# Kernel optimization log

Measured on AMD Instinct MI355X. Metric: run time of the kernel, lower is better.

Reference implementation:

```python
import jax, jax.numpy as jnp
import numpy as np

E = 1024   # embed_dim
H = 16     # num_heads
D = E // H # head_dim = 64
B = 2
S = 2048

def setup_inputs() -> dict:
    key = jax.random.key(0)
    ks = jax.random.split(key, 11)
    std = 0.02
    return {
        "query": jax.random.normal(ks[0], (B, S, E), jnp.float32),
        "key":   jax.random.normal(ks[1], (B, S, E), jnp.float32),
        "value": jax.random.normal(ks[2], (B, S, E), jnp.float32),
        "Wq": std * jax.random.normal(ks[3], (E, E), jnp.float32),
        "bq": jnp.zeros((E,), jnp.float32),
        "Wk": std * jax.random.normal(ks[4], (D, E), jnp.float32),
        "bk": jnp.zeros((D,), jnp.float32),
        "Wv": std * jax.random.normal(ks[5], (D, E), jnp.float32),
        "bv": jnp.zeros((D,), jnp.float32),
        "Wo": std * jax.random.normal(ks[6], (E, E), jnp.float32),
        "bo": jnp.zeros((E,), jnp.float32),
    }

def reference(query, key, value, Wq, bq, Wk, bk, Wv, bv, Wo, bo):
    b, t, _ = query.shape
    scaling = D ** -0.5
    q = query @ Wq.T + bq                      # [B, T, E]
    k = key @ Wk.T + bk                        # [B, S, D] (single shared KV head)
    v = value @ Wv.T + bv                      # [B, S, D]
    q = q.reshape(b, t, H, D).transpose(0, 2, 1, 3) * scaling  # [B, H, T, D]
    # MQA: broadcast shared k/v across heads inside einsum (no materialized expand)
    attn_weights = jnp.einsum("bhtd,bsd->bhts", q, k)          # [B, H, T, S]
    attn_probs = jax.nn.softmax(attn_weights, axis=-1)
    attn_output = jnp.einsum("bhts,bsd->bhtd", attn_probs, v)  # [B, H, T, D]
    attn_output = attn_output.transpose(0, 2, 1, 3).reshape(b, t, E)
    return attn_output @ Wo.T + bo
```

## Files before the change

### kernel.cpp

```cpp
#include <hip/hip_runtime.h>

#define E_DIM  1024
#define H_HEADS 16
#define D_HEAD  64
#define B_BATCH 2
#define S_SEQ  2048
#define M_ROWS (B_BATCH * S_SEQ)

typedef unsigned short u16;
typedef unsigned int   u32;
typedef __attribute__((ext_vector_type(8))) short bf16x8;
typedef __attribute__((ext_vector_type(4))) short bf16x4;
typedef __attribute__((ext_vector_type(4))) float f32x4;

#define MFMA32(a, b, c) __builtin_amdgcn_mfma_f32_16x16x32_bf16(a, b, c, 0, 0, 0)

#if __has_builtin(__builtin_amdgcn_mfma_f32_16x16x16bf16_1k)
#define HAVE_MFMA16 1
#define MFMA16(a, b, c) __builtin_amdgcn_mfma_f32_16x16x16bf16_1k(a, b, c, 0, 0, 0)
#else
#define HAVE_MFMA16 0
#endif

__device__ __forceinline__ u16 f2bf(float f) {
    union { float f; u32 i; } x; x.f = f;
    u32 r = x.i + 0x7fffu + ((x.i >> 16) & 1u);
    return (u16)(r >> 16);
}

#if __has_builtin(__builtin_amdgcn_cvt_pk_bf16_f32)
typedef __attribute__((ext_vector_type(2))) __bf16 bfp2;
__device__ __forceinline__ u32 pk2(float a, float b) {
    bfp2 t = __builtin_amdgcn_cvt_pk_bf16_f32(a, b);
    union { bfp2 v; u32 u; } c; c.v = t; return c.u;
}
#else
__device__ __forceinline__ u32 pk2(float a, float b) {
    return (u32)f2bf(a) | ((u32)f2bf(b) << 16);
}
#endif

__device__ __forceinline__ bf16x8 cvt8(const float4& a, const float4& b) {
    union { u32 u[4]; bf16x8 v; } t;
    t.u[0] = pk2(a.x, a.y); t.u[1] = pk2(a.z, a.w);
    t.u[2] = pk2(b.x, b.y); t.u[3] = pk2(b.z, b.w);
    return t.v;
}
__device__ __forceinline__ bf16x4 pack4(const f32x4& v) {
    union { u32 u[2]; bf16x4 w; } t;
    t.u[0] = pk2(v[0], v[1]); t.u[1] = pk2(v[2], v[3]);
    return t.w;
}

__device__ __forceinline__ void gl_lds16(const u16* g, u16* l) {
    __builtin_amdgcn_global_load_lds(
        (const __attribute__((address_space(1))) u32*)g,
        (__attribute__((address_space(3))) u32*)l, 16, 0, 0);
}

__global__ __launch_bounds__(256) void prep_kernel(
    const float* __restrict__ query, const float* __restrict__ Wq,
    const float* __restrict__ Wo,
    u16* __restrict__ qc, u16* __restrict__ wq_bf, u16* __restrict__ wo_bf,
    const float* __restrict__ key, const float* __restrict__ value,
    const float* __restrict__ Wk, const float* __restrict__ Wv,
    const float* __restrict__ bk, const float* __restrict__ bv,
    u16* __restrict__ Kout, u16* __restrict__ VTout, int M, int K)
{
    __shared__ u16 Asm[2][64 * 32];
    __shared__ u16 Bsm[2][64 * 32];

    const int bid = blockIdx.x;
    const int tid = threadIdx.x;

    if (bid >= 128) {
        const int cbid = bid - 128;
        const float* src; u16* dst; size_t base;
        if (cbid < 2048)      { src = query; dst = qc;    base = (size_t)cbid * 2048; }
        else if (cbid < 2560) { src = Wq;    dst = wq_bf; base = (size_t)(cbid - 2048) * 2048; }
        else                  { src = Wo;    dst = wo_bf; base = (size_t)(cbid - 2560) * 2048; }
        const size_t i = base + (size_t)tid * 8;
        float4 a = ((const float4*)(src + i))[0];
        float4 b = ((const float4*)(src + i))[1];
        *(bf16x8*)(dst + i) = cvt8(a, b);
        return;
    }

    const bool vproj = (bid >= 64);
    const float* A    = vproj ? value : key;
    const float* W    = vproj ? Wv : Wk;
    const float* bias = vproj ? bv : bk;

    const int w  = tid >> 6;
    const int ln = tid & 63;
    const int n  = ln & 15;
    const int qd = ln >> 4;
    const int wm = (w & 1) * 32;
    const int wn = (w >> 1) * 32;
    const int m0 = (bid & 63) * 64;

    const int srow = tid >> 2;
    const int scol = (tid & 3) * 8;

    f32x4 acc[2][2];
#pragma unroll
    for (int mt = 0; mt < 2; mt++)
#pragma unroll
        for (int nt = 0; nt < 2; nt++) acc[mt][nt] = (f32x4){0.f, 0.f, 0.f, 0.f};

    float4 a0, a1, w0, w1;
    auto loadT = [&](int k0) {
        const float* pa = A + (size_t)(m0 + srow) * K + k0 + scol;
        const float* pw = W + (size_t)srow * K + k0 + scol;
        a0 = ((const float4*)pa)[0]; a1 = ((const float4*)pa)[1];
        w0 = ((const float4*)pw)[0]; w1 = ((const float4*)pw)[1];
    };

    const int nk = K / 32;
    loadT(0);
    *(bf16x8*)&Asm[0][srow * 32 + scol] = cvt8(a0, a1);
    *(bf16x8*)&Bsm[0][srow * 32 + scol] = cvt8(w0, w1);

    for (int t = 0; t < nk; ++t) {
        if (t + 1 < nk) loadT((t + 1) * 32);
        __syncthreads();

        bf16x8 af[2], bfr[2];
#pragma unroll
        for (int t2 = 0; t2 < 2; t2++) {
            af[t2]  = *(const bf16x8*)&Asm[t & 1][(wm + t2 * 16 + n) * 32 + qd * 8];
            bfr[t2] = *(const bf16x8*)&Bsm[t & 1][(wn + t2 * 16 + n) * 32 + qd * 8];
        }
#pragma unroll
        for (int mt = 0; mt < 2; mt++)
#pragma unroll
            for (int nt = 0; nt < 2; nt++)
                acc[mt][nt] = MFMA32(af[mt], bfr[nt], acc[mt][nt]);

        if (t + 1 < nk) {
            *(bf16x8*)&Asm[(t + 1) & 1][srow * 32 + scol] = cvt8(a0, a1);
            *(bf16x8*)&Bsm[(t + 1) & 1][srow * 32 + scol] = cvt8(w0, w1);
        }
    }

    if (!vproj) {
#pragma unroll
        for (int mt = 0; mt < 2; mt++)
#pragma unroll
            for (int r = 0; r < 4; r++) {
                const int row = m0 + wm + mt * 16 + qd * 4 + r;
#pragma unroll
                for (int nt = 0; nt < 2; nt++) {
                    const int col = wn + nt * 16 + n;
                    Kout[(size_t)row * 64 + col] = f2bf(acc[mt][nt][r] + bias[col]);
                }
            }
    } else {
#pragma unroll
        for (int mt = 0; mt < 2; mt++)
#pragma unroll
            for (int nt = 0; nt < 2; nt++) {
                const int col = wn + nt * 16 + n;
                const int row0 = m0 + wm + mt * 16 + qd * 4;
                float b4 = bias[col];
                ushort4 pk;
                pk.x = f2bf(acc[mt][nt][0] + b4);
                pk.y = f2bf(acc[mt][nt][1] + b4);
                pk.z = f2bf(acc[mt][nt][2] + b4);
                pk.w = f2bf(acc[mt][nt][3] + b4);
                *(ushort4*)&VTout[(size_t)col * M + row0] = pk;
            }
    }
}

template<bool OUT_BF16>
__global__ __launch_bounds__(256, 2) void gemm_bf16_kernel(
    const u16* __restrict__ A, const u16* __restrict__ W,
    const float* __restrict__ bias, void* __restrict__ Cv,
    int M, int N, int K, float scale)
{
    __shared__ u16 Asm[3][2][128 * 32];
    __shared__ u16 Bsm[3][2][64 * 32];

    const int tid = threadIdx.x;
    const int w  = tid >> 6;
    const int ln = tid & 63;
    const int n  = ln & 15;
    const int qd = ln >> 4;
    const int ns = (n & 3) ^ (n >> 2);
    const int wm = (w & 1) * 64;
    const int wn = (w >> 1) * 32;

    const int m0 = blockIdx.y * 128;
    const int n0 = blockIdx.x * 64;

    const int srow = tid >> 2;
    const int sblk = tid & 3;
    const int sc   = ((sblk ^ (srow & 3) ^ ((srow >> 2) & 3)) * 8);

    f32x4 acc[4][2];
#pragma unroll
    for (int mt = 0; mt < 4; mt++)
#pragma unroll
        for (int nt = 0; nt < 2; nt++) acc[mt][nt] = (f32x4){0.f, 0.f, 0.f, 0.f};

    auto stage = [&](int p, int k0) {
#pragma unroll
        for (int kb = 0; kb < 2; kb++)
#pragma unroll
            for (int g = 0; g < 2; g++) {
                const int row = g * 64 + srow;
                gl_lds16(A + (size_t)(m0 + row) * K + k0 + kb * 32 + sc,
                         &Asm[p][kb][row * 32 + sblk * 8]);
            }
#pragma unroll
        for (int kb = 0; kb < 2; kb++)
            gl_lds16(W + (size_t)(n0 + srow) * K + k0 + kb * 32 + sc,
                     &Bsm[p][kb][srow * 32 + sblk * 8]);
    };
    auto compute = [&](int p) {
        bf16x8 af[4][2], bfr[2][2];
#pragma unroll
        for (int kb = 0; kb < 2; kb++) {
#pragma unroll
            for (int mt = 0; mt < 4; mt++) {
                const int r = wm + mt * 16 + n;
                af[mt][kb] = *(const bf16x8*)&Asm[p][kb][r * 32 + ((qd ^ ns) * 8)];
            }
#pragma unroll
            for (int nt = 0; nt < 2; nt++) {
                const int r = wn + nt * 16 + n;
                bfr[nt][kb] = *(const bf16x8*)&Bsm[p][kb][r * 32 + ((qd ^ ns) * 8)];
            }
        }
#pragma unroll
        for (int kb = 0; kb < 2; kb++)
#pragma unroll
            for (int mt = 0; mt < 4; mt++)
#pragma unroll
                for (int nt = 0; nt < 2; nt++)
                    acc[mt][nt] = MFMA32(af[mt][kb], bfr[nt][kb], acc[mt][nt]);
    };

    const int nt_tiles = K / 64;
    stage(0, 0);
    stage(1, 64);

    int pc = 0, ps = 2;
    for (int t = 0; t + 2 < nt_tiles; ++t) {
        asm volatile("s_waitcnt vmcnt(6)" ::: "memory");
        __builtin_amdgcn_s_barrier();
        __builtin_amdgcn_sched_barrier(0);
        stage(ps, (t + 2) * 64);
        compute(pc);
        pc = (pc == 2) ? 0 : pc + 1;
        ps = (ps == 2) ? 0 : ps + 1;
    }
    asm volatile("s_waitcnt vmcnt(6)" ::: "memory");
    __builtin_amdgcn_s_barrier();
    __builtin_amdgcn_sched_barrier(0);
    compute(pc);
    pc = (pc == 2) ? 0 : pc + 1;
    asm volatile("s_waitcnt vmcnt(0)" ::: "memory");
    __builtin_amdgcn_s_barrier();
    __builtin_amdgcn_sched_barrier(0);
    compute(pc);

    float bb[2];
#pragma unroll
    for (int nt = 0; nt < 2; nt++) bb[nt] = bias[n0 + wn + nt * 16 + n] * scale;

#pragma unroll
    for (int mt = 0; mt < 4; mt++)
#pragma unroll
        for (int r = 0; r < 4; r++) {
            const int row = m0 + wm + mt * 16 + qd * 4 + r;
#pragma unroll
            for (int nt = 0; nt < 2; nt++) {
                const int col = n0 + wn + nt * 16 + n;
                float v = acc[mt][nt][r] * scale + bb[nt];
                if (OUT_BF16) ((u16*)Cv)[(size_t)row * N + col] = f2bf(v);
                else        ((float*)Cv)[(size_t)row * N + col] = v;
            }
        }
}

__global__ __launch_bounds__(256, 2) void mqa_attn_fused_kernel(
    const u16* __restrict__ QC, const u16* __restrict__ WQ,
    const float* __restrict__ bq,
    const u16* __restrict__ Kt, const u16* __restrict__ VT,
    u16* __restrict__ O, float scaling)
{
    __shared__ u16 lds[32768];
#if !HAVE_MFMA16
    __shared__ u16 psm[4][32 * 128];
#endif

    const int tid = threadIdx.x;
    const int w   = tid >> 6;
    const int ln  = tid & 63;
    const int n   = ln & 15;
    const int qd  = ln >> 4;
    const int lr  = ln >> 2;
    const int blk = ln & 3;
    const int ns  = (n & 3) ^ (n >> 2);
    const int rs  = (lr & 3) ^ (lr >> 2);

    const int bid = blockIdx.x;
    const int qb = bid & 15;
    const int h  = (bid >> 4) & (H_HEADS - 1);
    const int b  = bid >> 8;
    const int q0 = qb * 128;

    const u16* ag = QC + (size_t)(b * S_SEQ + q0) * E_DIM;
    const u16* wg = WQ + (size_t)(h * 64) * E_DIM;

    const int srow = tid >> 2;
    const int sblk = tid & 3;
    const int sc   = ((sblk ^ (srow & 3) ^ ((srow >> 2) & 3)) * 8);

    auto stageP1 = [&](int buf, int k0) {
        u16* pa = lds + buf * 12288;
        u16* pb = pa + 8192;
#pragma unroll
        for (int kb = 0; kb < 2; kb++)
#pragma unroll
            for (int g = 0; g < 2; g++) {
                const int row = g * 64 + srow;
                gl_lds16(ag + (size_t)row * E_DIM + k0 + kb * 32 + sc,
                         pa + kb * 4096 + row * 32 + sblk * 8);
            }
#pragma unroll
        for (int kb = 0; kb < 2; kb++)
            gl_lds16(wg + (size_t)srow * E_DIM + k0 + kb * 32 + sc,
                     pb + kb * 2048 + srow * 32 + sblk * 8);
    };

    float bqv[4];
#pragma unroll
    for (int nt = 0; nt < 4; nt++) bqv[nt] = bq[h * 64 + nt * 16 + n] * scaling;

    f32x4 qacc[2][4];
#pragma unroll
    for (int mt = 0; mt < 2; mt++)
#pragma unroll
        for (int nt = 0; nt < 4; nt++) qacc[mt][nt] = (f32x4){0.f, 0.f, 0.f, 0.f};

    stageP1(0, 0);
    for (int t = 0; t < 16; ++t) {
        __syncthreads();
        if (t + 1 < 16) stageP1((t + 1) & 1, (t + 1) * 64);
        const u16* pa = lds + (t & 1) * 12288;
        const u16* pb = pa + 8192;
        bf16x8 af[2][2], bfr[4][2];
#pragma unroll
        for (int kb = 0; kb < 2; kb++) {
#pragma unroll
            for (int mt = 0; mt < 2; mt++) {
                const int r = w * 32 + mt * 16 + n;
                af[mt][kb] = *(const bf16x8*)&pa[kb * 4096 + r * 32 + ((qd ^ ns) * 8)];
            }
#pragma unroll
            for (int nt = 0; nt < 4; nt++) {
                const int r = nt * 16 + n;
                bfr[nt][kb] = *(const bf16x8*)&pb[kb * 2048 + r * 32 + ((qd ^ ns) * 8)];
            }
        }
#pragma unroll
        for (int kb = 0; kb < 2; kb++)
#pragma unroll
            for (int mt = 0; mt < 2; mt++)
#pragma unroll
                for (int nt = 0; nt < 4; nt++)
                    qacc[mt][nt] = MFMA32(af[mt][kb], bfr[nt][kb], qacc[mt][nt]);
    }

    {
        u16* qsm = lds + 24576;
#pragma unroll
        for (int mt = 0; mt < 2; mt++)
#pragma unroll
            for (int r = 0; r < 4; r++) {
                const int row = w * 32 + mt * 16 + qd * 4 + r;
                const int rsw = (row & 3) ^ ((row >> 2) & 3);
#pragma unroll
                for (int nt = 0; nt < 4; nt++) {
                    const int col = nt * 16 + n;
                    float v = qacc[mt][nt][r] * scaling + bqv[nt];
                    const int kb = col >> 5, c = col & 31;
                    qsm[kb * 4096 + row * 32 + (((c >> 3) ^ rsw) * 8) + (c & 7)] = f2bf(v);
                }
            }
    }
    __syncthreads();

    bf16x8 qa[2][2];
#pragma unroll
    for (int mt = 0; mt < 2; mt++)
#pragma unroll
        for (int kb = 0; kb < 2; kb++) {
            const int row = w * 32 + mt * 16 + n;
            qa[mt][kb] = *(const bf16x8*)&lds[24576 + kb * 4096 + row * 32 + ((qd ^ ns) * 8)];
        }

    const u16* kg = Kt + (size_t)b * S_SEQ * 64;
    const u16* vg = VT + (size_t)b * S_SEQ;

    auto KSM = [&](int p, int kb) -> u16* { return lds + ((p * 2 + kb) * 4096); };
    auto VSM = [&](int p, int c)  -> u16* { return lds + 16384 + ((p * 4 + c) * 2048); };

    auto stageKV = [&](int p, int s0) {
#pragma unroll
        for (int kb = 0; kb < 2; kb++)
#pragma unroll
            for (int j = 0; j < 2; j++) {
                const int row = w * 32 + j * 16 + lr;
                gl_lds16(kg + (size_t)(s0 + row) * 64 + kb * 32 + ((blk ^ rs) * 8),
                         KSM(p, kb) + row * 32 + blk * 8);
            }
#pragma unroll
        for (int j = 0; j < 4; j++) {
            const int d = j * 16 + lr;
            gl_lds16(vg + (size_t)d * M_ROWS + s0 + w * 32 + ((blk ^ rs) * 8),
                     VSM(p, w) + d * 32 + blk * 8);
        }
    };

    stageKV(0, 0);

    f32x4 acc_o[2][4];
    float lsum[2] = {0.f, 0.f};
#pragma unroll
    for (int mt = 0; mt < 2; mt++)
#pragma unroll
        for (int ntd = 0; ntd < 4; ntd++) acc_o[mt][ntd] = (f32x4){0.f, 0.f, 0.f, 0.f};

    int p = 0;
    for (int s0 = 0; s0 < S_SEQ; s0 += 128) {
        __syncthreads();
        if (s0 + 128 < S_SEQ) stageKV(p ^ 1, s0 + 128);

        f32x4 sacc[2][8];
#pragma unroll
        for (int mt = 0; mt < 2; mt++)
#pragma unroll
            for (int nt = 0; nt < 8; nt++) sacc[mt][nt] = (f32x4){0.f, 0.f, 0.f, 0.f};
#pragma unroll
        for (int nt = 0; nt < 8; nt++) {
            const int rowk = nt * 16 + n;
#pragma unroll
            for (int kb = 0; kb < 2; kb++) {
                bf16x8 kf = *(const bf16x8*)&KSM(p, kb)[rowk * 32 + ((qd ^ ns) * 8)];
                sacc[0][nt] = MFMA32(kf, qa[0][kb], sacc[0][nt]);
                sacc[1][nt] = MFMA32(kf, qa[1][kb], sacc[1][nt]);
            }
        }

        bf16x4 pa[2][8];
#pragma unroll
        for (int mt = 0; mt < 2; mt++) {
            float ls = 0.f;
#pragma unroll
            for (int nt = 0; nt < 8; nt++) {
#pragma unroll
                for (int r = 0; r < 4; r++) {
                    float pv = exp2f(sacc[mt][nt][r]);
                    sacc[mt][nt][r] = pv;
                    ls += pv;
                }
                pa[mt][nt] = pack4(sacc[mt][nt]);
            }
            lsum[mt] += ls;
        }

#if HAVE_MFMA16
#pragma unroll
        for (int kk = 0; kk < 8; kk++) {
            const int c = kk >> 1;
            const int lblk = (kk & 1) * 2 + (qd >> 1);
#pragma unroll
            for (int ntd = 0; ntd < 4; ntd++) {
                const int d = ntd * 16 + n;
                bf16x4 bv = *(const bf16x4*)
                    &VSM(p, c)[d * 32 + ((lblk ^ ns) * 8) + (qd & 1) * 4];
                acc_o[0][ntd] = MFMA16(pa[0][kk], bv, acc_o[0][ntd]);
                acc_o[1][ntd] = MFMA16(pa[1][kk], bv, acc_o[1][ntd]);
            }
        }
#else
#pragma unroll
        for (int mt = 0; mt < 2; mt++)
#pragma unroll
            for (int nt = 0; nt < 8; nt++) {
                const int t = mt * 16 + n;
                const int lb = nt * 2 + (qd >> 1);
                union { bf16x4 v; uint2 u; } pw; pw.v = pa[mt][nt];
                *(uint2*)&psm[w][t * 128 + ((lb ^ n) * 8) + (qd & 1) * 4] = pw.u;
            }
        __syncthreads();
#pragma unroll
        for (int kb = 0; kb < 4; kb++) {
            bf16x8 paf[2];
#pragma unroll
            for (int mt = 0; mt < 2; mt++) {
                const int t = mt * 16 + n;
                paf[mt] = *(const bf16x8*)&psm[w][t * 128 + (((kb * 4 + qd) ^ n) * 8)];
            }
#pragma unroll
            for (int ntd = 0; ntd < 4; ntd++) {
                const int d = ntd * 16 + n;
                bf16x8 bv = *(const bf16x8*)&VSM(p, kb)[d * 32 + ((qd ^ ns) * 8)];
                acc_o[0][ntd] = MFMA32(paf[0], bv, acc_o[0][ntd]);
                acc_o[1][ntd] = MFMA32(paf[1], bv, acc_o[1][ntd]);
            }
        }
#endif
        p ^= 1;
    }

#pragma unroll
    for (int mt = 0; mt < 2; mt++) {
        lsum[mt] += __shfl_xor(lsum[mt], 16);
        lsum[mt] += __shfl_xor(lsum[mt], 32);
    }
#pragma unroll
    for (int mt = 0; mt < 2; mt++)
#pragma unroll
        for (int r = 0; r < 4; r++) {
            float inv = 1.f / __shfl(lsum[mt], qd * 4 + r);
            const int grow = b * S_SEQ + q0 + w * 32 + mt * 16 + qd * 4 + r;
#pragma unroll
            for (int ntd = 0; ntd < 4; ntd++) {
                const int gcol = h * D_HEAD + ntd * 16 + n;
                O[(size_t)grow * E_DIM + gcol] = f2bf(acc_o[mt][ntd][r] * inv);
            }
        }
}

extern "C" void kernel_launch(void* const* d_in, const int* in_sizes, int n_in,
                              void* d_out, int out_size, void* d_ws, size_t ws_size,
                              hipStream_t stream) {
    const float* query = (const float*)d_in[0];
    const float* key   = (const float*)d_in[1];
    const float* value = (const float*)d_in[2];
    const float* Wq    = (const float*)d_in[3];
    const float* bq    = (const float*)d_in[4];
    const float* Wk    = (const float*)d_in[5];
    const float* bk    = (const float*)d_in[6];
    const float* Wv    = (const float*)d_in[7];
    const float* bv    = (const float*)d_in[8];
    const float* Wo    = (const float*)d_in[9];
    const float* bo    = (const float*)d_in[10];
    float* out = (float*)d_out;

    const int M = M_ROWS;

    u16* q_bf  = (u16*)d_ws;
    u16* k_bf  = q_bf + (size_t)M * E_DIM;
    u16* vt_bf = k_bf + (size_t)M * D_HEAD;
    u16* wq_bf = vt_bf + (size_t)M * D_HEAD;
    u16* wo_bf = wq_bf + (size_t)E_DIM * E_DIM;

    u16* qc_bf = (u16*)d_out;

    dim3 blk(256);
    const float scaling = 0.125f * 1.44269504088896f;

    prep_kernel<<<dim3(3200), blk, 0, stream>>>(
        query, Wq, Wo, qc_bf, wq_bf, wo_bf,
        key, value, Wk, Wv, bk, bv, k_bf, vt_bf, M, E_DIM);

    mqa_attn_fused_kernel<<<dim3(512), blk, 0, stream>>>(
        qc_bf, wq_bf, bq, k_bf, vt_bf, q_bf, scaling);

    gemm_bf16_kernel<false><<<dim3(E_DIM / 64, M / 128), blk, 0, stream>>>(
        q_bf, wo_bf, bo, out, M, E_DIM, E_DIM, 1.0f);
}
```

Before: 235.5 us.

## Fuse fp32-to-bf16 conversion of query, Wq and Wo into consumer kernels

Drops the separate conversion pass that wrote bf16 copies of query, Wq and Wo. The attention kernel now loads fp32 query and Wq into registers and converts them while writing to LDS. The output GEMM does the same for fp32 Wo. The KV projection kernel moves to a 2D grid and loses its double buffering. This removes one kernel launch and the write/re-read of converted buffers. In exchange, the heavily reused fp32 operands double the global load bytes. It also replaces the async global-to-LDS loads and the three-stage pipeline with register-staged double buffering.

```diff
diff --git a/kernel.cpp b/kernel.cpp
--- a/kernel.cpp
+++ b/kernel.cpp
@@ -58,46 +58,28 @@
         (__attribute__((address_space(3))) u32*)l, 16, 0, 0);
 }
 
-__global__ __launch_bounds__(256) void prep_kernel(
-    const float* __restrict__ query, const float* __restrict__ Wq,
-    const float* __restrict__ Wo,
-    u16* __restrict__ qc, u16* __restrict__ wq_bf, u16* __restrict__ wo_bf,
+__global__ __launch_bounds__(256) void kv_proj_kernel(
     const float* __restrict__ key, const float* __restrict__ value,
     const float* __restrict__ Wk, const float* __restrict__ Wv,
     const float* __restrict__ bk, const float* __restrict__ bv,
     u16* __restrict__ Kout, u16* __restrict__ VTout, int M, int K)
 {
-    __shared__ u16 Asm[2][64 * 32];
-    __shared__ u16 Bsm[2][64 * 32];
-
-    const int bid = blockIdx.x;
-    const int tid = threadIdx.x;
-
-    if (bid >= 128) {
-        const int cbid = bid - 128;
-        const float* src; u16* dst; size_t base;
-        if (cbid < 2048)      { src = query; dst = qc;    base = (size_t)cbid * 2048; }
-        else if (cbid < 2560) { src = Wq;    dst = wq_bf; base = (size_t)(cbid - 2048) * 2048; }
-        else                  { src = Wo;    dst = wo_bf; base = (size_t)(cbid - 2560) * 2048; }
-        const size_t i = base + (size_t)tid * 8;
-        float4 a = ((const float4*)(src + i))[0];
-        float4 b = ((const float4*)(src + i))[1];
-        *(bf16x8*)(dst + i) = cvt8(a, b);
-        return;
-    }
-
-    const bool vproj = (bid >= 64);
+    const bool vproj = (blockIdx.y == 1);
     const float* A    = vproj ? value : key;
     const float* W    = vproj ? Wv : Wk;
     const float* bias = vproj ? bv : bk;
 
+    __shared__ u16 Asm[64 * 32];
+    __shared__ u16 Bsm[64 * 32];
+
+    const int tid = threadIdx.x;
     const int w  = tid >> 6;
     const int ln = tid & 63;
     const int n  = ln & 15;
     const int qd = ln >> 4;
     const int wm = (w & 1) * 32;
     const int wn = (w >> 1) * 32;
-    const int m0 = (bid & 63) * 64;
+    const int m0 = blockIdx.x * 64;
 
     const int srow = tid >> 2;
     const int scol = (tid & 3) * 8;
@@ -108,39 +90,27 @@
 #pragma unroll
         for (int nt = 0; nt < 2; nt++) acc[mt][nt] = (f32x4){0.f, 0.f, 0.f, 0.f};
 
-    float4 a0, a1, w0, w1;
-    auto loadT = [&](int k0) {
+    for (int k0 = 0; k0 < K; k0 += 32) {
+        __syncthreads();
         const float* pa = A + (size_t)(m0 + srow) * K + k0 + scol;
         const float* pw = W + (size_t)srow * K + k0 + scol;
-        a0 = ((const float4*)pa)[0]; a1 = ((const float4*)pa)[1];
-        w0 = ((const float4*)pw)[0]; w1 = ((const float4*)pw)[1];
-    };
-
-    const int nk = K / 32;
-    loadT(0);
-    *(bf16x8*)&Asm[0][srow * 32 + scol] = cvt8(a0, a1);
-    *(bf16x8*)&Bsm[0][srow * 32 + scol] = cvt8(w0, w1);
-
-    for (int t = 0; t < nk; ++t) {
-        if (t + 1 < nk) loadT((t + 1) * 32);
+        float4 a0 = ((const float4*)pa)[0], a1 = ((const float4*)pa)[1];
+        float4 w0 = ((const float4*)pw)[0], w1 = ((const float4*)pw)[1];
+        *(bf16x8*)&Asm[srow * 32 + scol] = cvt8(a0, a1);
+        *(bf16x8*)&Bsm[srow * 32 + scol] = cvt8(w0, w1);
         __syncthreads();
 
         bf16x8 af[2], bfr[2];
 #pragma unroll
-        for (int t2 = 0; t2 < 2; t2++) {
-            af[t2]  = *(const bf16x8*)&Asm[t & 1][(wm + t2 * 16 + n) * 32 + qd * 8];
-            bfr[t2] = *(const bf16x8*)&Bsm[t & 1][(wn + t2 * 16 + n) * 32 + qd * 8];
+        for (int t = 0; t < 2; t++) {
+            af[t]  = *(const bf16x8*)&Asm[(wm + t * 16 + n) * 32 + qd * 8];
+            bfr[t] = *(const bf16x8*)&Bsm[(wn + t * 16 + n) * 32 + qd * 8];
         }
 #pragma unroll
         for (int mt = 0; mt < 2; mt++)
 #pragma unroll
             for (int nt = 0; nt < 2; nt++)
                 acc[mt][nt] = MFMA32(af[mt], bfr[nt], acc[mt][nt]);
-
-        if (t + 1 < nk) {
-            *(bf16x8*)&Asm[(t + 1) & 1][srow * 32 + scol] = cvt8(a0, a1);
-            *(bf16x8*)&Bsm[(t + 1) & 1][srow * 32 + scol] = cvt8(w0, w1);
-        }
     }
 
     if (!vproj) {
@@ -173,14 +143,13 @@
     }
 }
 
-template<bool OUT_BF16>
-__global__ __launch_bounds__(256, 2) void gemm_bf16_kernel(
-    const u16* __restrict__ A, const u16* __restrict__ W,
-    const float* __restrict__ bias, void* __restrict__ Cv,
-    int M, int N, int K, float scale)
+__global__ __launch_bounds__(256, 2) void ogemm_kernel(
+    const u16* __restrict__ A, const float* __restrict__ Wo,
+    const float* __restrict__ bias, float* __restrict__ C,
+    int M, int N, int K)
 {
-    __shared__ u16 Asm[3][2][128 * 32];
-    __shared__ u16 Bsm[3][2][64 * 32];
+    __shared__ u16 Asm[2][2][128 * 32];
+    __shared__ u16 Bsm[2][2][64 * 32];
 
     const int tid = threadIdx.x;
     const int w  = tid >> 6;
@@ -204,7 +173,8 @@
 #pragma unroll
         for (int nt = 0; nt < 2; nt++) acc[mt][nt] = (f32x4){0.f, 0.f, 0.f, 0.f};
 
-    auto stage = [&](int p, int k0) {
+    float4 wreg[2][2];
+    auto stageA = [&](int p, int k0) {
 #pragma unroll
         for (int kb = 0; kb < 2; kb++)
 #pragma unroll
@@ -213,10 +183,19 @@
                 gl_lds16(A + (size_t)(m0 + row) * K + k0 + kb * 32 + sc,
                          &Asm[p][kb][row * 32 + sblk * 8]);
             }
+    };
+    auto loadW = [&](int k0) {
+#pragma unroll
+        for (int kb = 0; kb < 2; kb++) {
+            const float* pw = Wo + (size_t)(n0 + srow) * K + k0 + kb * 32 + sc;
+            wreg[kb][0] = ((const float4*)pw)[0];
+            wreg[kb][1] = ((const float4*)pw)[1];
+        }
+    };
+    auto writeW = [&](int p) {
 #pragma unroll
         for (int kb = 0; kb < 2; kb++)
-            gl_lds16(W + (size_t)(n0 + srow) * K + k0 + kb * 32 + sc,
-                     &Bsm[p][kb][srow * 32 + sblk * 8]);
+            *(bf16x8*)&Bsm[p][kb][srow * 32 + sblk * 8] = cvt8(wreg[kb][0], wreg[kb][1]);
     };
     auto compute = [&](int p) {
         bf16x8 af[4][2], bfr[2][2];
@@ -242,33 +221,23 @@
                     acc[mt][nt] = MFMA32(af[mt][kb], bfr[nt][kb], acc[mt][nt]);
     };
 
-    const int nt_tiles = K / 64;
-    stage(0, 0);
-    stage(1, 64);
-
-    int pc = 0, ps = 2;
-    for (int t = 0; t + 2 < nt_tiles; ++t) {
-        asm volatile("s_waitcnt vmcnt(6)" ::: "memory");
-        __builtin_amdgcn_s_barrier();
-        __builtin_amdgcn_sched_barrier(0);
-        stage(ps, (t + 2) * 64);
-        compute(pc);
-        pc = (pc == 2) ? 0 : pc + 1;
-        ps = (ps == 2) ? 0 : ps + 1;
-    }
-    asm volatile("s_waitcnt vmcnt(6)" ::: "memory");
-    __builtin_amdgcn_s_barrier();
-    __builtin_amdgcn_sched_barrier(0);
-    compute(pc);
-    pc = (pc == 2) ? 0 : pc + 1;
-    asm volatile("s_waitcnt vmcnt(0)" ::: "memory");
-    __builtin_amdgcn_s_barrier();
-    __builtin_amdgcn_sched_barrier(0);
-    compute(pc);
+    stageA(0, 0); loadW(0); writeW(0);
+
+    int p = 0;
+    for (int k0 = 64; k0 < K; k0 += 64) {
+        __syncthreads();
+        stageA(p ^ 1, k0);
+        loadW(k0);
+        compute(p);
+        writeW(p ^ 1);
+        p ^= 1;
+    }
+    __syncthreads();
+    compute(p);
 
     float bb[2];
 #pragma unroll
-    for (int nt = 0; nt < 2; nt++) bb[nt] = bias[n0 + wn + nt * 16 + n] * scale;
+    for (int nt = 0; nt < 2; nt++) bb[nt] = bias[n0 + wn + nt * 16 + n];
 
 #pragma unroll
     for (int mt = 0; mt < 4; mt++)
@@ -278,15 +247,13 @@
 #pragma unroll
             for (int nt = 0; nt < 2; nt++) {
                 const int col = n0 + wn + nt * 16 + n;
-                float v = acc[mt][nt][r] * scale + bb[nt];
-                if (OUT_BF16) ((u16*)Cv)[(size_t)row * N + col] = f2bf(v);
-                else        ((float*)Cv)[(size_t)row * N + col] = v;
+                C[(size_t)row * N + col] = acc[mt][nt][r] + bb[nt];
             }
         }
 }
 
 __global__ __launch_bounds__(256, 2) void mqa_attn_fused_kernel(
-    const u16* __restrict__ QC, const u16* __restrict__ WQ,
+    const float* __restrict__ QF, const float* __restrict__ WQ,
     const float* __restrict__ bq,
     const u16* __restrict__ Kt, const u16* __restrict__ VT,
     u16* __restrict__ O, float scaling)
@@ -312,28 +279,41 @@
     const int b  = bid >> 8;
     const int q0 = qb * 128;
 
-    const u16* ag = QC + (size_t)(b * S_SEQ + q0) * E_DIM;
-    const u16* wg = WQ + (size_t)(h * 64) * E_DIM;
+    const float* ag = QF + (size_t)(b * S_SEQ + q0) * E_DIM;
+    const float* wg = WQ + (size_t)(h * 64) * E_DIM;
 
     const int srow = tid >> 2;
     const int sblk = tid & 3;
     const int sc   = ((sblk ^ (srow & 3) ^ ((srow >> 2) & 3)) * 8);
 
-    auto stageP1 = [&](int buf, int k0) {
+    float4 areg[2][2][2];
+    float4 breg[2][2];
+    auto loadP1 = [&](int k0) {
+#pragma unroll
+        for (int kb = 0; kb < 2; kb++) {
+#pragma unroll
+            for (int g = 0; g < 2; g++) {
+                const float* pa = ag + (size_t)(g * 64 + srow) * E_DIM + k0 + kb * 32 + sc;
+                areg[kb][g][0] = ((const float4*)pa)[0];
+                areg[kb][g][1] = ((const float4*)pa)[1];
+            }
+            const float* pw = wg + (size_t)srow * E_DIM + k0 + kb * 32 + sc;
+            breg[kb][0] = ((const float4*)pw)[0];
+            breg[kb][1] = ((const float4*)pw)[1];
+        }
+    };
+    auto writeP1 = [&](int buf) {
         u16* pa = lds + buf * 12288;
         u16* pb = pa + 8192;
 #pragma unroll
-        for (int kb = 0; kb < 2; kb++)
-#pragma unroll
-            for (int g = 0; g < 2; g++) {
-                const int row = g * 64 + srow;
-                gl_lds16(ag + (size_t)row * E_DIM + k0 + kb * 32 + sc,
-                         pa + kb * 4096 + row * 32 + sblk * 8);
-            }
-#pragma unroll
-        for (int kb = 0; kb < 2; kb++)
-            gl_lds16(wg + (size_t)srow * E_DIM + k0 + kb * 32 + sc,
-                     pb + kb * 2048 + srow * 32 + sblk * 8);
+        for (int kb = 0; kb < 2; kb++) {
+#pragma unroll
+            for (int g = 0; g < 2; g++)
+                *(bf16x8*)&pa[kb * 4096 + (g * 64 + srow) * 32 + sblk * 8] =
+                    cvt8(areg[kb][g][0], areg[kb][g][1]);
+            *(bf16x8*)&pb[kb * 2048 + srow * 32 + sblk * 8] =
+                cvt8(breg[kb][0], breg[kb][1]);
+        }
     };
 
     float bqv[4];
@@ -346,10 +326,10 @@
 #pragma unroll
         for (int nt = 0; nt < 4; nt++) qacc[mt][nt] = (f32x4){0.f, 0.f, 0.f, 0.f};
 
-    stageP1(0, 0);
+    loadP1(0); writeP1(0);
     for (int t = 0; t < 16; ++t) {
         __syncthreads();
-        if (t + 1 < 16) stageP1((t + 1) & 1, (t + 1) * 64);
+        if (t + 1 < 16) loadP1((t + 1) * 64);
         const u16* pa = lds + (t & 1) * 12288;
         const u16* pb = pa + 8192;
         bf16x8 af[2][2], bfr[4][2];
@@ -373,6 +353,7 @@
 #pragma unroll
                 for (int nt = 0; nt < 4; nt++)
                     qacc[mt][nt] = MFMA32(af[mt][kb], bfr[nt][kb], qacc[mt][nt]);
+        if (t + 1 < 16) writeP1((t + 1) & 1);
     }
 
     {
@@ -558,21 +539,16 @@
     u16* q_bf  = (u16*)d_ws;
     u16* k_bf  = q_bf + (size_t)M * E_DIM;
     u16* vt_bf = k_bf + (size_t)M * D_HEAD;
-    u16* wq_bf = vt_bf + (size_t)M * D_HEAD;
-    u16* wo_bf = wq_bf + (size_t)E_DIM * E_DIM;
-
-    u16* qc_bf = (u16*)d_out;
 
     dim3 blk(256);
     const float scaling = 0.125f * 1.44269504088896f;
 
-    prep_kernel<<<dim3(3200), blk, 0, stream>>>(
-        query, Wq, Wo, qc_bf, wq_bf, wo_bf,
+    kv_proj_kernel<<<dim3(M / 64, 2), blk, 0, stream>>>(
         key, value, Wk, Wv, bk, bv, k_bf, vt_bf, M, E_DIM);
 
     mqa_attn_fused_kernel<<<dim3(512), blk, 0, stream>>>(
-        qc_bf, wq_bf, bq, k_bf, vt_bf, q_bf, scaling);
-
-    gemm_bf16_kernel<false><<<dim3(E_DIM / 64, M / 128), blk, 0, stream>>>(
-        q_bf, wo_bf, bo, out, M, E_DIM, E_DIM, 1.0f);
-}
+        query, Wq, bq, k_bf, vt_bf, q_bf, scaling);
+
+    ogemm_kernel<<<dim3(E_DIM / 64, M / 128), blk, 0, stream>>>(
+        q_bf, Wo, bo, out, M, E_DIM, E_DIM);
+}
```

Measured after the change: 251.9 us. +7.0%, slower.
